# Kernel tuning notes

Hardware: AMD Instinct MI355X
Metric: run time of the kernel (lower is better)

Reference implementation:

```python
import jax, jax.numpy as jnp
import numpy as np

WINDOWS = (5, 5, 25, 25)  # per-layer neighborhood window sizes
N_HEAD = 4


def _na2d(x, wqkv, bqkv, wo, bo, window, n_head):
    """2D neighborhood (NATTEN-style) attention, channels-last x: [B,H,W,C].
    Each query attends to a window x window neighborhood whose start is
    clamped so the window stays inside the image (NATTEN boundary rule)."""
    B, H, W, C = x.shape
    hd = C // n_head
    qkv = x @ wqkv + bqkv                      # [B,H,W,3C]
    q, k, v = jnp.split(qkv, 3, axis=-1)
    q = q.reshape(B, H, W, n_head, hd) * (hd ** -0.5)
    k = k.reshape(B, H, W, n_head, hd)
    v = v.reshape(B, H, W, n_head, hd)
    half = window // 2
    sh = jnp.clip(jnp.arange(H) - half, 0, H - window)   # window start per row
    sw = jnp.clip(jnp.arange(W) - half, 0, W - window)
    ih = sh[:, None] + jnp.arange(window)                # [H, window]
    iw = sw[:, None] + jnp.arange(window)                # [W, window]
    # gather K/V neighborhoods -> [B,H,W,window,window,n_head,hd]
    kn = k[:, ih[:, None, :, None], iw[None, :, None, :]]
    vn = v[:, ih[:, None, :, None], iw[None, :, None, :]]
    scores = jnp.einsum('bhwnd,bhwijnd->bhwnij', q, kn)
    kk = window * window
    att = jax.nn.softmax(scores.reshape(B, H, W, n_head, kk), axis=-1)
    out = jnp.einsum('bhwnk,bhwknd->bhwnd', att,
                     vn.reshape(B, H, W, kk, n_head, hd))
    return out.reshape(B, H, W, C) @ wo + bo


def setup_inputs() -> dict:
    key = jax.random.key(0)
    ks = jax.random.split(key, 5)
    B, T, F, C = 1, 64, 352, 24   # batch, time frames, CQT bins (88*4), n_unit
    L = len(WINDOWS)
    s = 1.0 / np.sqrt(C)
    return {
        'x': jax.random.normal(ks[0], (B, T, F, C), jnp.float32),
        'qkv_w': jax.random.normal(ks[1], (L, C, 3 * C), jnp.float32) * s,
        'qkv_b': jax.random.normal(ks[2], (L, 3 * C), jnp.float32) * 0.01,
        'out_w': jax.random.normal(ks[3], (L, C, C), jnp.float32) * s,
        'out_b': jax.random.normal(ks[4], (L, C), jnp.float32) * 0.01,
    }


def reference(x, qkv_w, qkv_b, out_w, out_b):
    for i, win in enumerate(WINDOWS):
        res = x
        x = _na2d(x, qkv_w[i], qkv_b[i], out_w[i], out_b[i], win, N_HEAD) + res
        if i < 2:
            # F.max_pool2d(kernel=(2,1)) on (B,H,W,C) layout pools the W dim by 2
            B, H, W, C = x.shape
            x = x.reshape(B, H, W // 2, 2, C).max(axis=3)
    return jnp.swapaxes(x, -2, -1)   # x.transpose(-2, -1)
```

## Files before the change

### kernel.cpp

```cpp
#include <hip/hip_runtime.h>
#include <cstdint>

#define QSCALE 0.40824829046386301636f

__global__ __launch_bounds__(256) void qkv_first(
    const float* __restrict__ x, const float* __restrict__ w,
    const float* __restrict__ b, float* __restrict__ q,
    float* __restrict__ kv, int npx)
{
  __shared__ __align__(16) float swT[72 * 24];
  __shared__ float sb[72];
  for (int i = threadIdx.x; i < 1728; i += 256) swT[(i % 72) * 24 + i / 72] = w[i];
  if (threadIdx.x < 72) sb[threadIdx.x] = b[threadIdx.x];
  __syncthreads();
  const int t = blockIdx.x * 256 + threadIdx.x;
  const int p = t >> 2, jg = t & 3;
  if (p >= npx) return;
  float xr[24];
  const float4* xp = (const float4*)(x + (size_t)p * 24);
#pragma unroll
  for (int i = 0; i < 6; ++i) {
    const float4 f = xp[i];
    xr[4*i] = f.x; xr[4*i+1] = f.y; xr[4*i+2] = f.z; xr[4*i+3] = f.w;
  }
#pragma unroll
  for (int jj = 0; jj < 18; ++jj) {
    const int j = jg * 18 + jj;
    const float* wr = &swT[j * 24];
    float acc = sb[j];
#pragma unroll
    for (int c = 0; c < 24; ++c) acc += xr[c] * wr[c];
    if (j < 24)      q[((size_t)(j / 6) * npx + p) * 6 + j % 6] = acc * QSCALE;
    else if (j < 48) { const int u = j - 24; kv[((size_t)(u / 6) * npx + p) * 12 + u % 6] = acc; }
    else             { const int u = j - 48; kv[((size_t)(u / 6) * npx + p) * 12 + 6 + u % 6] = acc; }
  }
}

__global__ __launch_bounds__(128) void attn5(
    const float* __restrict__ q, const float* __restrict__ kv,
    float* __restrict__ att, int H, int W)
{
  __shared__ __align__(16) float skv[12 * 12 * 12];
  const int tid = threadIdx.x;
  const int h0 = blockIdx.y * 8, w0 = blockIdx.x * 8, hd = blockIdx.z;
  const int N = H * W;
  const int rlo = min(max(h0 - 2, 0), H - 5);
  const int nr  = min(max(h0 + 5, 0), H - 5) + 4 - rlo + 1;
  const int clo = min(max(w0 - 2, 0), W - 5);
  const int nc  = min(max(w0 + 5, 0), W - 5) + 4 - clo + 1;
  const float* kvh = kv + (size_t)hd * N * 12;
  const int ncc = nc * 3;
  for (int i = tid; i < nr * ncc; i += 128) {
    const int r = i / ncc, c4 = i - r * ncc;
    const float4 v = ((const float4*)(kvh + ((size_t)(rlo + r) * W + clo) * 12))[c4];
    ((float4*)skv)[r * 36 + c4] = v;
  }
  __syncthreads();

  const int ql = tid >> 1, sr = tid & 1;
  const int qh = h0 + (ql >> 3), qw = w0 + (ql & 7);
  const float* qp = q + ((size_t)hd * N + (size_t)qh * W + qw) * 6;
  const float q0 = qp[0], q1 = qp[1], q2 = qp[2], q3 = qp[3], q4 = qp[4], q5 = qp[5];
  const int shq = min(max(qh - 2, 0), H - 5) - rlo;
  const int swq = min(max(qw - 2, 0), W - 5) - clo;

  float m = -1e30f, l = 0.f, a0 = 0, a1 = 0, a2 = 0, a3 = 0, a4 = 0, a5 = 0;
  for (int rr = sr; rr < 5; rr += 2) {
    const float* rowp = skv + ((shq + rr) * 12 + swq) * 12;
#pragma unroll
    for (int cc = 0; cc < 5; ++cc) {
      const float* p = rowp + cc * 12;
      const float4 A = *(const float4*)p;
      const float4 B = *(const float4*)(p + 4);
      const float4 C = *(const float4*)(p + 8);
      const float s = q0*A.x + q1*A.y + q2*A.z + q3*A.w + q4*B.x + q5*B.y;
      float d = s - m;
      if (d > 8.0f) {
        const float r2 = __expf(-d);
        l *= r2; a0 *= r2; a1 *= r2; a2 *= r2; a3 *= r2; a4 *= r2; a5 *= r2;
        m = s; d = 0.f;
      }
      const float e = __expf(d);
      l += e;
      a0 += e*B.z; a1 += e*B.w; a2 += e*C.x;
      a3 += e*C.y; a4 += e*C.z; a5 += e*C.w;
    }
  }
  {
    const float om = __shfl_xor(m, 1), ol = __shfl_xor(l, 1);
    const float o0 = __shfl_xor(a0, 1), o1 = __shfl_xor(a1, 1), o2 = __shfl_xor(a2, 1);
    const float o3 = __shfl_xor(a3, 1), o4 = __shfl_xor(a4, 1), o5 = __shfl_xor(a5, 1);
    const float nm = fmaxf(m, om);
    const float f1 = __expf(m - nm), f2 = __expf(om - nm);
    l = l*f1 + ol*f2;
    a0 = a0*f1 + o0*f2; a1 = a1*f1 + o1*f2; a2 = a2*f1 + o2*f2;
    a3 = a3*f1 + o3*f2; a4 = a4*f1 + o4*f2; a5 = a5*f1 + o5*f2;
  }
  if (sr == 0) {
    const float inv = 1.0f / l;
    float* ap = att + ((size_t)qh * W + qw) * 24 + hd * 6;
    ((float2*)ap)[0] = make_float2(a0*inv, a1*inv);
    ((float2*)ap)[1] = make_float2(a2*inv, a3*inv);
    ((float2*)ap)[2] = make_float2(a4*inv, a5*inv);
  }
}

__global__ __launch_bounds__(256) void attn25(
    const float* __restrict__ q, const float* __restrict__ kv,
    float* __restrict__ att)
{
  constexpr int H = 64, W = 88, N = H * W;
  __shared__ __align__(16) float skv[28 * 32 * 12];
  const int tid = threadIdx.x;
  const int h0 = blockIdx.y * 4, w0 = blockIdx.x * 8, hd = blockIdx.z;
  const int rlo = min(max(h0 - 12, 0), H - 25);
  const int nr  = min(max(h0 + 3 - 12, 0), H - 25) + 24 - rlo + 1;
  const int clo = min(max(w0 - 12, 0), W - 25);
  const int nc  = min(max(w0 + 7 - 12, 0), W - 25) + 24 - clo + 1;
  const float* kvh = kv + (size_t)hd * N * 12;
  const int ncc = nc * 3;
  for (int i = tid; i < nr * ncc; i += 256) {
    const int r = i / ncc, c4 = i - r * ncc;
    const float4 v = ((const float4*)(kvh + ((size_t)(rlo + r) * W + clo) * 12))[c4];
    ((float4*)skv)[r * 96 + c4] = v;
  }
  __syncthreads();

  const int ql = tid >> 3, s = tid & 7, sr = s >> 2, sc = s & 3;
  const int qh = h0 + (ql >> 3), qw = w0 + (ql & 7);
  const float* qp = q + ((size_t)hd * N + (size_t)qh * W + qw) * 6;
  const float q0 = qp[0], q1 = qp[1], q2 = qp[2], q3 = qp[3], q4 = qp[4], q5 = qp[5];
  const int shq = min(max(qh - 12, 0), H - 25) - rlo;
  const int swq = min(max(qw - 12, 0), W - 25) - clo;

  float m = -1e30f, l = 0.f, a0 = 0, a1 = 0, a2 = 0, a3 = 0, a4 = 0, a5 = 0;
  for (int rr = sr; rr < 25; rr += 2) {
    const float* rowp = skv + ((shq + rr) * 32 + swq) * 12;
    for (int cc = sc; cc < 25; cc += 4) {
      const float* p = rowp + cc * 12;
      const float4 A = *(const float4*)p;
      const float4 B = *(const float4*)(p + 4);
      const float4 C = *(const float4*)(p + 8);
      const float s2 = q0*A.x + q1*A.y + q2*A.z + q3*A.w + q4*B.x + q5*B.y;
      float d = s2 - m;
      if (d > 8.0f) {
        const float r2 = __expf(-d);
        l *= r2; a0 *= r2; a1 *= r2; a2 *= r2; a3 *= r2; a4 *= r2; a5 *= r2;
        m = s2; d = 0.f;
      }
      const float e = __expf(d);
      l += e;
      a0 += e*B.z; a1 += e*B.w; a2 += e*C.x;
      a3 += e*C.y; a4 += e*C.z; a5 += e*C.w;
    }
  }
#pragma unroll
  for (int mask = 1; mask <= 4; mask <<= 1) {
    const float om = __shfl_xor(m, mask), ol = __shfl_xor(l, mask);
    const float o0 = __shfl_xor(a0, mask), o1 = __shfl_xor(a1, mask), o2 = __shfl_xor(a2, mask);
    const float o3 = __shfl_xor(a3, mask), o4 = __shfl_xor(a4, mask), o5 = __shfl_xor(a5, mask);
    const float nm = fmaxf(m, om);
    const float f1 = __expf(m - nm), f2 = __expf(om - nm);
    m = nm;
    l = l*f1 + ol*f2;
    a0 = a0*f1 + o0*f2; a1 = a1*f1 + o1*f2; a2 = a2*f1 + o2*f2;
    a3 = a3*f1 + o3*f2; a4 = a4*f1 + o4*f2; a5 = a5*f1 + o5*f2;
  }
  if (s == 0) {
    const float inv = 1.0f / l;
    float* ap = att + ((size_t)qh * W + qw) * 24 + hd * 6;
    ((float2*)ap)[0] = make_float2(a0*inv, a1*inv);
    ((float2*)ap)[1] = make_float2(a2*inv, a3*inv);
    ((float2*)ap)[2] = make_float2(a4*inv, a5*inv);
  }
}

__global__ __launch_bounds__(256) void glue_pool(
    const float* __restrict__ att, const float* __restrict__ xres,
    const float* __restrict__ wo, const float* __restrict__ bo,
    const float* __restrict__ wq, const float* __restrict__ bq,
    float* __restrict__ xn, float* __restrict__ qn, float* __restrict__ kvn,
    int Nn)
{
  __shared__ __align__(16) float swoT[24 * 24];
  __shared__ float sbo[24];
  __shared__ __align__(16) float swqT[72 * 24];
  __shared__ float sbq[72];
  __shared__ __align__(16) float sy[128 * 28];
  const int tid = threadIdx.x;
  for (int i = tid; i < 576; i += 256) swoT[(i % 24) * 24 + i / 24] = wo[i];
  for (int i = tid; i < 1728; i += 256) swqT[(i % 72) * 24 + i / 72] = wq[i];
  if (tid < 24) sbo[tid] = bo[tid];
  if (tid < 72) sbq[tid] = bq[tid];
  __syncthreads();

  {
    const int lpx = tid >> 1, half = tid & 1;
    const size_t spx = (size_t)blockIdx.x * 128 + lpx;
    float ar[24];
    const float4* ap = (const float4*)(att + spx * 24);
#pragma unroll
    for (int i = 0; i < 6; ++i) {
      const float4 f = ap[i];
      ar[4*i] = f.x; ar[4*i+1] = f.y; ar[4*i+2] = f.z; ar[4*i+3] = f.w;
    }
    float res[12];
    const float4* rp = (const float4*)(xres + spx * 24 + half * 12);
#pragma unroll
    for (int i = 0; i < 3; ++i) {
      const float4 f = rp[i];
      res[4*i] = f.x; res[4*i+1] = f.y; res[4*i+2] = f.z; res[4*i+3] = f.w;
    }
#pragma unroll
    for (int k = 0; k < 12; ++k) {
      const int c = half * 12 + k;
      const float* wr = &swoT[c * 24];
      float acc = sbo[c] + res[k];
#pragma unroll
      for (int j = 0; j < 24; ++j) acc += ar[j] * wr[j];
      sy[lpx * 28 + c] = acc;
    }
  }
  __syncthreads();
  {
    const int ppl = tid >> 2, jg = tid & 3;
    const size_t gp = (size_t)blockIdx.x * 64 + ppl;
    float xp[24];
    const float* y0 = &sy[(2 * ppl) * 28];
    const float* y1 = &sy[(2 * ppl + 1) * 28];
#pragma unroll
    for (int c = 0; c < 24; ++c) xp[c] = fmaxf(y0[c], y1[c]);
    if (jg == 0) {
      float4* xo = (float4*)(xn + gp * 24);
#pragma unroll
      for (int i = 0; i < 6; ++i)
        xo[i] = make_float4(xp[4*i], xp[4*i+1], xp[4*i+2], xp[4*i+3]);
    }
#pragma unroll
    for (int jj = 0; jj < 18; ++jj) {
      const int j = jg * 18 + jj;
      const float* wr = &swqT[j * 24];
      float acc = sbq[j];
#pragma unroll
      for (int c = 0; c < 24; ++c) acc += xp[c] * wr[c];
      if (j < 24)      qn[((size_t)(j / 6) * Nn + gp) * 6 + j % 6] = acc * QSCALE;
      else if (j < 48) { const int u = j - 24; kvn[((size_t)(u / 6) * Nn + gp) * 12 + u % 6] = acc; }
      else             { const int u = j - 48; kvn[((size_t)(u / 6) * Nn + gp) * 12 + 6 + u % 6] = acc; }
    }
  }
}

__global__ __launch_bounds__(256) void glue_nopool(
    const float* __restrict__ att, const float* __restrict__ xres,
    const float* __restrict__ wo, const float* __restrict__ bo,
    const float* __restrict__ wq, const float* __restrict__ bq,
    float* __restrict__ xn, float* __restrict__ qn, float* __restrict__ kvn,
    int Nn)
{
  __shared__ __align__(16) float swoT[24 * 24];
  __shared__ float sbo[24];
  __shared__ __align__(16) float swqT[72 * 24];
  __shared__ float sbq[72];
  __shared__ __align__(16) float sy[64 * 28];
  const int tid = threadIdx.x;
  for (int i = tid; i < 576; i += 256) swoT[(i % 24) * 24 + i / 24] = wo[i];
  for (int i = tid; i < 1728; i += 256) swqT[(i % 72) * 24 + i / 72] = wq[i];
  if (tid < 24) sbo[tid] = bo[tid];
  if (tid < 72) sbq[tid] = bq[tid];
  __syncthreads();

  {
    const int lpx = tid >> 2, qt = tid & 3;
    const size_t spx = (size_t)blockIdx.x * 64 + lpx;
    float ar[24];
    const float4* ap = (const float4*)(att + spx * 24);
#pragma unroll
    for (int i = 0; i < 6; ++i) {
      const float4 f = ap[i];
      ar[4*i] = f.x; ar[4*i+1] = f.y; ar[4*i+2] = f.z; ar[4*i+3] = f.w;
    }
#pragma unroll
    for (int k = 0; k < 6; ++k) {
      const int c = qt * 6 + k;
      const float* wr = &swoT[c * 24];
      float acc = sbo[c] + xres[spx * 24 + c];
#pragma unroll
      for (int j = 0; j < 24; ++j) acc += ar[j] * wr[j];
      sy[lpx * 28 + c] = acc;
      xn[spx * 24 + c] = acc;
    }
  }
  __syncthreads();
  {
    const int lpx = tid >> 2, jg = tid & 3;
    const size_t gp = (size_t)blockIdx.x * 64 + lpx;
    const float* yr = &sy[lpx * 28];
    float xp[24];
#pragma unroll
    for (int c = 0; c < 24; ++c) xp[c] = yr[c];
#pragma unroll
    for (int jj = 0; jj < 18; ++jj) {
      const int j = jg * 18 + jj;
      const float* wr = &swqT[j * 24];
      float acc = sbq[j];
#pragma unroll
      for (int c = 0; c < 24; ++c) acc += xp[c] * wr[c];
      if (j < 24)      qn[((size_t)(j / 6) * Nn + gp) * 6 + j % 6] = acc * QSCALE;
      else if (j < 48) { const int u = j - 24; kvn[((size_t)(u / 6) * Nn + gp) * 12 + u % 6] = acc; }
      else             { const int u = j - 48; kvn[((size_t)(u / 6) * Nn + gp) * 12 + 6 + u % 6] = acc; }
    }
  }
}

__global__ __launch_bounds__(256) void final_out(
    const float* __restrict__ att, const float* __restrict__ xres,
    const float* __restrict__ wo, const float* __restrict__ bo,
    float* __restrict__ dout)
{
  __shared__ __align__(16) float swoT[24 * 24];
  __shared__ float sbo[24];
  const int tid = threadIdx.x;
  for (int i = tid; i < 576; i += 256) swoT[(i % 24) * 24 + i / 24] = wo[i];
  if (tid < 24) sbo[tid] = bo[tid];
  __syncthreads();
  const int lpx = tid >> 1, half = tid & 1;
  const size_t spx = (size_t)blockIdx.x * 128 + lpx;
  const int gh = (int)(spx / 88), gw = (int)(spx % 88);
  float ar[24];
  const float4* ap = (const float4*)(att + spx * 24);
#pragma unroll
  for (int i = 0; i < 6; ++i) {
    const float4 f = ap[i];
    ar[4*i] = f.x; ar[4*i+1] = f.y; ar[4*i+2] = f.z; ar[4*i+3] = f.w;
  }
  float res[12];
  const float4* rp = (const float4*)(xres + spx * 24 + half * 12);
#pragma unroll
  for (int i = 0; i < 3; ++i) {
    const float4 f = rp[i];
    res[4*i] = f.x; res[4*i+1] = f.y; res[4*i+2] = f.z; res[4*i+3] = f.w;
  }
#pragma unroll
  for (int k = 0; k < 12; ++k) {
    const int c = half * 12 + k;
    const float* wr = &swoT[c * 24];
    float acc = sbo[c] + res[k];
#pragma unroll
    for (int j = 0; j < 24; ++j) acc += ar[j] * wr[j];
    dout[((size_t)gh * 24 + c) * 88 + gw] = acc;
  }
}

extern "C" void kernel_launch(void* const* d_in, const int* in_sizes, int n_in,
                              void* d_out, int out_size, void* d_ws, size_t ws_size,
                              hipStream_t stream)
{
  const float* x      = (const float*)d_in[0];
  const float* qkv_w  = (const float*)d_in[1];
  const float* qkv_b  = (const float*)d_in[2];
  const float* out_w  = (const float*)d_in[3];
  const float* out_b  = (const float*)d_in[4];
  float* out = (float*)d_out;
  float* ws = (float*)d_ws;

  const int N0 = 64 * 352, N1 = 64 * 176, N2 = 64 * 88;
  float* q   = ws;
  float* kvb = q + (size_t)N0 * 24;
  float* att = kvb + (size_t)N0 * 48;
  float* x1  = att + (size_t)N0 * 24;
  float* x2  = x1 + (size_t)N1 * 24;
  float* x3  = x2 + (size_t)N2 * 24;

  qkv_first<<<(N0 * 4) / 256, 256, 0, stream>>>(x, qkv_w, qkv_b, q, kvb, N0);

  attn5<<<dim3(44, 8, 4), 128, 0, stream>>>(q, kvb, att, 64, 352);
  glue_pool<<<176, 256, 0, stream>>>(att, x, out_w, out_b,
                                     qkv_w + 1728, qkv_b + 72, x1, q, kvb, N1);

  attn5<<<dim3(22, 8, 4), 128, 0, stream>>>(q, kvb, att, 64, 176);
  glue_pool<<<88, 256, 0, stream>>>(att, x1, out_w + 576, out_b + 24,
                                    qkv_w + 2 * 1728, qkv_b + 2 * 72, x2, q, kvb, N2);

  attn25<<<dim3(11, 16, 4), 256, 0, stream>>>(q, kvb, att);
  glue_nopool<<<88, 256, 0, stream>>>(att, x2, out_w + 2 * 576, out_b + 2 * 24,
                                      qkv_w + 3 * 1728, qkv_b + 3 * 72, x3, q, kvb, N2);

  attn25<<<dim3(11, 16, 4), 256, 0, stream>>>(q, kvb, att);
  final_out<<<44, 256, 0, stream>>>(att, x3, out_w + 3 * 576, out_b + 3 * 24, out);
}
```

Before: 165.1 us.

## Share K/V loads across four query rows in window-25 attention kernel

The window-25 attention kernel now assigns one 32-lane group per query column covering all four query rows of the tile. Each K/V element read from shared memory is reused for up to four queries, with a predicate checking whether the row lies inside each query's window. The shared-memory row stride is padded to 388 floats, presumably to avoid bank conflicts. The cost is more registers for four sets of online-softmax state, a wider 32-lane shuffle reduction, and divergence from the per-query row predicate.

```diff
diff --git a/kernel.cpp b/kernel.cpp
--- a/kernel.cpp
+++ b/kernel.cpp
@@ -110,7 +110,8 @@
     float* __restrict__ att)
 {
   constexpr int H = 64, W = 88, N = H * W;
-  __shared__ __align__(16) float skv[28 * 32 * 12];
+  constexpr int RS = 388;
+  __shared__ __align__(16) float skv[28 * RS];
   const int tid = threadIdx.x;
   const int h0 = blockIdx.y * 4, w0 = blockIdx.x * 8, hd = blockIdx.z;
   const int rlo = min(max(h0 - 12, 0), H - 25);
@@ -122,56 +123,86 @@
   for (int i = tid; i < nr * ncc; i += 256) {
     const int r = i / ncc, c4 = i - r * ncc;
     const float4 v = ((const float4*)(kvh + ((size_t)(rlo + r) * W + clo) * 12))[c4];
-    ((float4*)skv)[r * 96 + c4] = v;
-  }
-  __syncthreads();
-
-  const int ql = tid >> 3, s = tid & 7, sr = s >> 2, sc = s & 3;
-  const int qh = h0 + (ql >> 3), qw = w0 + (ql & 7);
-  const float* qp = q + ((size_t)hd * N + (size_t)qh * W + qw) * 6;
-  const float q0 = qp[0], q1 = qp[1], q2 = qp[2], q3 = qp[3], q4 = qp[4], q5 = qp[5];
-  const int shq = min(max(qh - 12, 0), H - 25) - rlo;
+    ((float4*)skv)[r * (RS / 4) + c4] = v;
+  }
+  __syncthreads();
+
+  const int qw_ = tid >> 5, slice = tid & 31, sr = slice >> 2, sc = slice & 3;
+  const int qw = w0 + qw_;
   const int swq = min(max(qw - 12, 0), W - 25) - clo;
 
-  float m = -1e30f, l = 0.f, a0 = 0, a1 = 0, a2 = 0, a3 = 0, a4 = 0, a5 = 0;
-  for (int rr = sr; rr < 25; rr += 2) {
-    const float* rowp = skv + ((shq + rr) * 32 + swq) * 12;
+  float qv[4][6];
+  int srel[4];
+#pragma unroll
+  for (int qi = 0; qi < 4; ++qi) {
+    const float* qp = q + ((size_t)hd * N + (size_t)(h0 + qi) * W + qw) * 6;
+#pragma unroll
+    for (int d = 0; d < 6; ++d) qv[qi][d] = qp[d];
+    srel[qi] = min(max(h0 + qi - 12, 0), H - 25) - rlo;
+  }
+
+  float m_[4], l_[4], acc[4][6];
+#pragma unroll
+  for (int qi = 0; qi < 4; ++qi) {
+    m_[qi] = -1e30f; l_[qi] = 0.f;
+#pragma unroll
+    for (int d = 0; d < 6; ++d) acc[qi][d] = 0.f;
+  }
+
+  for (int rg = sr; rg < nr; rg += 8) {
+    const float* rowp = skv + rg * RS + swq * 12;
     for (int cc = sc; cc < 25; cc += 4) {
       const float* p = rowp + cc * 12;
       const float4 A = *(const float4*)p;
       const float4 B = *(const float4*)(p + 4);
       const float4 C = *(const float4*)(p + 8);
-      const float s2 = q0*A.x + q1*A.y + q2*A.z + q3*A.w + q4*B.x + q5*B.y;
-      float d = s2 - m;
-      if (d > 8.0f) {
-        const float r2 = __expf(-d);
-        l *= r2; a0 *= r2; a1 *= r2; a2 *= r2; a3 *= r2; a4 *= r2; a5 *= r2;
-        m = s2; d = 0.f;
+#pragma unroll
+      for (int qi = 0; qi < 4; ++qi) {
+        if (rg >= srel[qi] && rg <= srel[qi] + 24) {
+          const float s = qv[qi][0]*A.x + qv[qi][1]*A.y + qv[qi][2]*A.z
+                        + qv[qi][3]*A.w + qv[qi][4]*B.x + qv[qi][5]*B.y;
+          float d = s - m_[qi];
+          if (d > 8.0f) {
+            const float r2 = __expf(-d);
+            l_[qi] *= r2;
+            acc[qi][0] *= r2; acc[qi][1] *= r2; acc[qi][2] *= r2;
+            acc[qi][3] *= r2; acc[qi][4] *= r2; acc[qi][5] *= r2;
+            m_[qi] = s; d = 0.f;
+          }
+          const float e = __expf(d);
+          l_[qi] += e;
+          acc[qi][0] += e*B.z; acc[qi][1] += e*B.w; acc[qi][2] += e*C.x;
+          acc[qi][3] += e*C.y; acc[qi][4] += e*C.z; acc[qi][5] += e*C.w;
+        }
       }
-      const float e = __expf(d);
-      l += e;
-      a0 += e*B.z; a1 += e*B.w; a2 += e*C.x;
-      a3 += e*C.y; a4 += e*C.z; a5 += e*C.w;
-    }
-  }
-#pragma unroll
-  for (int mask = 1; mask <= 4; mask <<= 1) {
-    const float om = __shfl_xor(m, mask), ol = __shfl_xor(l, mask);
-    const float o0 = __shfl_xor(a0, mask), o1 = __shfl_xor(a1, mask), o2 = __shfl_xor(a2, mask);
-    const float o3 = __shfl_xor(a3, mask), o4 = __shfl_xor(a4, mask), o5 = __shfl_xor(a5, mask);
-    const float nm = fmaxf(m, om);
-    const float f1 = __expf(m - nm), f2 = __expf(om - nm);
-    m = nm;
-    l = l*f1 + ol*f2;
-    a0 = a0*f1 + o0*f2; a1 = a1*f1 + o1*f2; a2 = a2*f1 + o2*f2;
-    a3 = a3*f1 + o3*f2; a4 = a4*f1 + o4*f2; a5 = a5*f1 + o5*f2;
-  }
-  if (s == 0) {
-    const float inv = 1.0f / l;
-    float* ap = att + ((size_t)qh * W + qw) * 24 + hd * 6;
-    ((float2*)ap)[0] = make_float2(a0*inv, a1*inv);
-    ((float2*)ap)[1] = make_float2(a2*inv, a3*inv);
-    ((float2*)ap)[2] = make_float2(a4*inv, a5*inv);
+    }
+  }
+
+#pragma unroll
+  for (int mask = 1; mask <= 16; mask <<= 1) {
+#pragma unroll
+    for (int qi = 0; qi < 4; ++qi) {
+      const float om = __shfl_xor(m_[qi], mask), ol = __shfl_xor(l_[qi], mask);
+      float oa[6];
+#pragma unroll
+      for (int d = 0; d < 6; ++d) oa[d] = __shfl_xor(acc[qi][d], mask);
+      const float nm = fmaxf(m_[qi], om);
+      const float f1 = __expf(m_[qi] - nm), f2 = __expf(om - nm);
+      m_[qi] = nm;
+      l_[qi] = l_[qi]*f1 + ol*f2;
+#pragma unroll
+      for (int d = 0; d < 6; ++d) acc[qi][d] = acc[qi][d]*f1 + oa[d]*f2;
+    }
+  }
+  if (slice == 0) {
+#pragma unroll
+    for (int qi = 0; qi < 4; ++qi) {
+      const float inv = 1.0f / l_[qi];
+      float* ap = att + ((size_t)(h0 + qi) * W + qw) * 24 + hd * 6;
+      ((float2*)ap)[0] = make_float2(acc[qi][0]*inv, acc[qi][1]*inv);
+      ((float2*)ap)[1] = make_float2(acc[qi][2]*inv, acc[qi][3]*inv);
+      ((float2*)ap)[2] = make_float2(acc[qi][4]*inv, acc[qi][5]*inv);
+    }
   }
 }
 
```

Result: slower. 176.1 us (+6.7%).
